# Kernel tuning notes

Measured on AMD Instinct MI355X. Metric: run time of the kernel, lower is better.

Reference implementation:

```python
import jax, jax.numpy as jnp
import numpy as np

N_NODES = 4096
N_EDGES = 16384
F_IN = 64
F_EDGE = 16
HID = 128
OUT = 64
N_GRAPHS = 32


def _encoder(x, edge_index, edge_attr, batch, p):
    N = x.shape[0]
    src, dst = edge_index[0], edge_index[1]
    # EdgeMLP: [E, F_edge] -> [E, F_in * HID] per-edge weight matrices
    h = jax.nn.relu(edge_attr @ p['e_w1'] + p['e_b1'])
    h = jax.nn.relu(h @ p['e_w2'] + p['e_b2'])
    Wmat = (h @ p['e_w3'] + p['e_b3']).reshape(-1, x.shape[1], p['root_w'].shape[1])  # [E, F_in, HID]
    # NNConv: message = x_src @ W_edge, scatter-add to dst, plus root transform + bias
    msg = jnp.einsum('ei,eio->eo', x[src], Wmat)  # [E, HID]
    agg = jax.ops.segment_sum(msg, dst, num_segments=N)
    h1 = jax.nn.relu(agg + x @ p['root_w'] + p['conv1_b'])  # [N, HID]
    # GATConv (1 head, concat=False) with self-loops (PyG default)
    loop = jnp.arange(N, dtype=src.dtype)
    si = jnp.concatenate([src, loop])
    di = jnp.concatenate([dst, loop])
    hp = h1 @ p['gat_w']  # [N, HID]
    a_s = hp @ p['att_src']  # [N]
    a_d = hp @ p['att_dst']  # [N]
    e = jax.nn.leaky_relu(a_s[si] + a_d[di], negative_slope=0.2)
    m = jax.ops.segment_max(e, di, num_segments=N)
    ex = jnp.exp(e - m[di])
    denom = jax.ops.segment_sum(ex, di, num_segments=N)
    alpha = ex / (denom[di] + 1e-16)
    h2 = jax.ops.segment_sum(alpha[:, None] * hp[si], di, num_segments=N) + p['gat_b']
    h2 = jax.nn.relu(h2)
    # global mean pool over graphs
    s = jax.ops.segment_sum(h2, batch, num_segments=N_GRAPHS)
    cnt = jax.ops.segment_sum(jnp.ones((N,), h2.dtype), batch, num_segments=N_GRAPHS)
    pooled = s / jnp.maximum(cnt, 1.0)[:, None]
    return jax.nn.relu(pooled @ p['fc1_w'] + p['fc1_b'])  # [B, OUT]


def setup_inputs() -> dict:
    key = jax.random.key(0)
    ks = jax.random.split(key, 24)
    d = {}
    d['x1'] = jax.random.normal(ks[0], (N_NODES, F_IN), jnp.float32)
    d['edge_index1'] = jax.random.randint(ks[1], (2, N_EDGES), 0, N_NODES)
    d['edge_attr1'] = jax.random.normal(ks[2], (N_EDGES, F_EDGE), jnp.float32)
    d['batch1'] = jnp.sort(jax.random.randint(ks[3], (N_NODES,), 0, N_GRAPHS))
    d['x2'] = jax.random.normal(ks[4], (N_NODES, F_IN), jnp.float32)
    d['edge_index2'] = jax.random.randint(ks[5], (2, N_EDGES), 0, N_NODES)
    d['edge_attr2'] = jax.random.normal(ks[6], (N_EDGES, F_EDGE), jnp.float32)
    d['batch2'] = jnp.sort(jax.random.randint(ks[7], (N_NODES,), 0, N_GRAPHS))

    def lin(k, fi, fo):
        return jax.random.normal(k, (fi, fo), jnp.float32) * (fi ** -0.5)

    d['e_w1'] = lin(ks[8], F_EDGE, 128); d['e_b1'] = jnp.zeros((128,), jnp.float32)
    d['e_w2'] = lin(ks[9], 128, 64); d['e_b2'] = jnp.zeros((64,), jnp.float32)
    d['e_w3'] = lin(ks[10], 64, F_IN * HID); d['e_b3'] = jnp.zeros((F_IN * HID,), jnp.float32)
    d['root_w'] = lin(ks[11], F_IN, HID); d['conv1_b'] = jnp.zeros((HID,), jnp.float32)
    d['gat_w'] = lin(ks[12], HID, HID)
    d['att_src'] = jax.random.normal(ks[13], (HID,), jnp.float32) * (HID ** -0.5)
    d['att_dst'] = jax.random.normal(ks[14], (HID,), jnp.float32) * (HID ** -0.5)
    d['gat_b'] = jnp.zeros((HID,), jnp.float32)
    d['fc1_w'] = lin(ks[15], HID, OUT); d['fc1_b'] = jnp.zeros((OUT,), jnp.float32)
    d['fc2_w'] = lin(ks[16], OUT, 1); d['fc2_b'] = jnp.zeros((1,), jnp.float32)
    return d


def reference(x1, edge_index1, edge_attr1, batch1, x2, edge_index2, edge_attr2, batch2,
              e_w1, e_b1, e_w2, e_b2, e_w3, e_b3, root_w, conv1_b,
              gat_w, att_src, att_dst, gat_b, fc1_w, fc1_b, fc2_w, fc2_b):
    p = dict(e_w1=e_w1, e_b1=e_b1, e_w2=e_w2, e_b2=e_b2, e_w3=e_w3, e_b3=e_b3,
             root_w=root_w, conv1_b=conv1_b, gat_w=gat_w, att_src=att_src,
             att_dst=att_dst, gat_b=gat_b, fc1_w=fc1_w, fc1_b=fc1_b,
             fc2_w=fc2_w, fc2_b=fc2_b)
    z1 = _encoder(x1, edge_index1, edge_attr1, batch1, p)
    z2 = _encoder(x2, edge_index2, edge_attr2, batch2, p)
    z = jnp.abs(z1 - z2) @ fc2_w + fc2_b  # [B, 1]
    return jax.nn.sigmoid(z).squeeze(1)  # [B]
```

## Files before the change

### kernel.cpp

```cpp
#include <hip/hip_runtime.h>
#include <hip/hip_bf16.h>
#include <math.h>

#define NN 4096
#define NE 16384
#define FIN 64
#define FE 16
#define HIDD 128
#define OUTD 64
#define NG 32
#define EP (NE + NN)
#define KSPLIT 2
#define NCH (64 / KSPLIT)

typedef __attribute__((ext_vector_type(4))) unsigned u4v;
typedef __attribute__((ext_vector_type(4))) float f4v;
typedef _Float16 f16x8 __attribute__((ext_vector_type(8)));

union FragH { u4v u; f16x8 h; };
union FH2 { _Float16 f[2]; unsigned u; };
union F16x8U { _Float16 f[8]; u4v u; };

__global__ void k_splitB(const float* __restrict__ w3, unsigned short* __restrict__ B1t) {
    __shared__ float lds[64 * 129];
    int c = blockIdx.x, t = threadIdx.x;
#pragma unroll
    for (int r = 0; r < 32; ++r) {
        int idx = r * 256 + t;
        lds[(idx >> 7) * 129 + (idx & 127)] = w3[(size_t)c * 8192 + idx];
    }
    __syncthreads();
#pragma unroll
    for (int r = 0; r < 32; ++r) {
        int e = r * 256 + t;
        float v = lds[(e & 63) * 129 + (e >> 6)];
        union { _Float16 f; unsigned short u; } cv;
        cv.f = (_Float16)v;
        B1t[(size_t)c * 8192 + e] = cv.u;
    }
}

#define PB_EMLP  4096
#define PB_BIAS  (PB_EMLP + 4096)
#define PB_TOTAL (PB_BIAS + 32)

__global__ void k_prep(const float* __restrict__ ea0, const float* __restrict__ ea1,
                       const float* __restrict__ w1, const float* __restrict__ b1,
                       const float* __restrict__ w2, const float* __restrict__ b2,
                       const float* __restrict__ X0, const float* __restrict__ X1,
                       const float* __restrict__ b3,
                       const int* __restrict__ ei0, const int* __restrict__ ei1,
                       float* __restrict__ h0, float* __restrict__ h1g,
                       float* __restrict__ Bb0, float* __restrict__ Bb1,
                       int* __restrict__ rowcnt) {
    int b = blockIdx.x, t = threadIdx.x;
    if (b < PB_EMLP) {
        int gi = b >> 11;
        int e0 = (b & 2047) * 8;
        const float* ea = gi ? ea1 : ea0;
        float* hout = gi ? h1g : h0;
        __shared__ float h1s[8][HIDD];
#pragma unroll
        for (int r = 0; r < 4; ++r) {
            int idx = r * 256 + t;
            int e1 = idx >> 7, j = idx & 127;
            float acc = b1[j];
#pragma unroll
            for (int i = 0; i < FE; ++i) acc += ea[(e0 + e1) * FE + i] * w1[i * HIDD + j];
            h1s[e1][j] = fmaxf(acc, 0.f);
        }
        __syncthreads();
#pragma unroll
        for (int r = 0; r < 2; ++r) {
            int idx = r * 256 + t;
            int e1 = idx >> 6, j = idx & 63;
            float acc = b2[j];
#pragma unroll 16
            for (int k = 0; k < HIDD; ++k) acc += h1s[e1][k] * w2[k * 64 + j];
            hout[(size_t)(e0 + e1) * 64 + j] = fmaxf(acc, 0.f);
        }
    } else if (b < PB_BIAS) {
        int bb = b - PB_EMLP;
        int gi = bb >> 11;
        int n = (bb & 2047) * 2 + (t >> 7);
        int o = t & 127;
        const float* X = gi ? X1 : X0;
        float* Bb = gi ? Bb1 : Bb0;
        float acc = 0.f;
#pragma unroll 16
        for (int i = 0; i < FIN; ++i) acc += X[n * FIN + i] * b3[i * HIDD + o];
        Bb[(size_t)n * HIDD + o] = acc;
    } else {
        int tid = (b - PB_BIAS) * 256 + t;
        for (int idx = tid; idx < 2 * EP; idx += 32 * 256) {
            int gi = idx / EP, e = idx % EP;
            const int* dst = (gi ? ei1 : ei0) + NE;
            int d = (e < NE) ? dst[e] : e - NE;
            atomicAdd(&rowcnt[gi * NN + d], 1);
        }
    }
}

__global__ void k_scan(const int* __restrict__ rowcnt, int* __restrict__ rowptr,
                       const int* __restrict__ batch0, const int* __restrict__ batch1,
                       int* __restrict__ br) {
    int b = blockIdx.x;
    if (b < 2) {
        int gi = b;
        const int* cnt = rowcnt + gi * NN;
        int* rp = rowptr + gi * (NN + 1);
        int t = threadIdx.x;
        int base = t * 4;
        int v0 = cnt[base], v1 = cnt[base + 1], v2 = cnt[base + 2], v3 = cnt[base + 3];
        int s = v0 + v1 + v2 + v3;
        __shared__ int sc[1024];
        sc[t] = s;
        __syncthreads();
        for (int off = 1; off < 1024; off <<= 1) {
            int a = (t >= off) ? sc[t - off] : 0;
            __syncthreads();
            sc[t] += a;
            __syncthreads();
        }
        int run = sc[t] - s;
        rp[base] = run; run += v0;
        rp[base + 1] = run; run += v1;
        rp[base + 2] = run; run += v2;
        rp[base + 3] = run; run += v3;
        if (t == 1023) rp[NN] = run;
    } else {
        int t = threadIdx.x;
        if (t < 66) {
            int gi = t / 33, g = t % 33;
            const int* batch = gi ? batch1 : batch0;
            int lo = 0, hi = NN;
            while (lo < hi) {
                int mid = (lo + hi) >> 1;
                if (batch[mid] < g) lo = mid + 1; else hi = mid;
            }
            br[gi * 33 + g] = lo;
        }
    }
}

__global__ void k_fill(const int* __restrict__ ei0, const int* __restrict__ ei1,
                       const int* __restrict__ rowptr, int* __restrict__ cnt2,
                       int* __restrict__ adj) {
    int idx = blockIdx.x * 256 + threadIdx.x;
    if (idx >= 2 * EP) return;
    int gi = idx / EP, e = idx % EP;
    const int* dst = (gi ? ei1 : ei0) + NE;
    int d = (e < NE) ? dst[e] : e - NE;
    int pos = rowptr[gi * (NN + 1) + d] + atomicAdd(&cnt2[gi * NN + d], 1);
    adj[gi * EP + pos] = e;
}

__global__ void __launch_bounds__(128, 2)
k_nnconv(const float* __restrict__ x0, const float* __restrict__ x1,
         const float* __restrict__ h_0, const float* __restrict__ h_1,
         const unsigned short* __restrict__ B1t,
         const float* __restrict__ Bb0, const float* __restrict__ Bb1,
         const int* __restrict__ ei0, const int* __restrict__ ei1,
         _Float16* __restrict__ msgh) {
    __shared__ __align__(16) float sm[32 * 128];
    int gi = blockIdx.z;
    const float* x = gi ? x1 : x0;
    const float* hh = gi ? h_1 : h_0;
    const float* Bb = gi ? Bb1 : Bb0;
    const int* src = gi ? ei1 : ei0;

    int t = threadIdx.x;
    int e0 = blockIdx.x * 64;
    int z = blockIdx.y;
    int ch = t >> 6;
    int l = t & 63, q4 = l >> 4, c16 = l & 15;

    FragH xf[4][2];
#pragma unroll
    for (int mf = 0; mf < 4; ++mf) {
        int s_ = src[e0 + mf * 16 + c16];
        const float* xr = &x[(size_t)s_ * FIN];
#pragma unroll
        for (int kf = 0; kf < 2; ++kf) {
            float xv[8];
            *(float4*)&xv[0] = *(const float4*)&xr[kf * 32 + q4 * 8];
            *(float4*)&xv[4] = *(const float4*)&xr[kf * 32 + q4 * 8 + 4];
            u4v w;
#pragma unroll
            for (int p = 0; p < 4; ++p) {
                FH2 c2;
                c2.f[0] = (_Float16)xv[2 * p];
                c2.f[1] = (_Float16)xv[2 * p + 1];
                w[p] = c2.u;
            }
            xf[mf][kf].u = w;
        }
    }

    f4v acc[4][4];
#pragma unroll
    for (int a = 0; a < 4; ++a)
#pragma unroll
        for (int b = 0; b < 4; ++b) acc[a][b] = (f4v){0.f, 0.f, 0.f, 0.f};

    const u4v* bp = (const u4v*)B1t;

#define LOADF(buf, cg)                                                          \
    {                                                                           \
        const u4v* cp = bp + (size_t)(cg) * 1024;                               \
        _Pragma("unroll") for (int kf = 0; kf < 2; ++kf)                        \
        _Pragma("unroll") for (int nf = 0; nf < 4; ++nf)                        \
            buf[kf * 4 + nf].u = cp[(ch * 64 + nf * 16 + c16) * 8 + kf * 4 + q4]; \
    }

#define DOMFMA(buf, COMP)                                                       \
    {                                                                           \
        _Pragma("unroll") for (int mf = 0; mf < 4; ++mf) {                      \
            FH2 hp2;                                                            \
            hp2.f[0] = (_Float16)hv4[mf].COMP;                                  \
            hp2.f[1] = hp2.f[0];                                                \
            unsigned hw = hp2.u;                                                \
            FragH hb; hb.u = (u4v){hw, hw, hw, hw};                             \
            _Pragma("unroll") for (int kf = 0; kf < 2; ++kf) {                  \
                FragH a1;                                                       \
                a1.h = hb.h * xf[mf][kf].h;                                     \
                _Pragma("unroll") for (int nf = 0; nf < 4; ++nf) {              \
                    acc[mf][nf] = __builtin_amdgcn_mfma_f32_16x16x32_f16(       \
                        a1.h, buf[kf * 4 + nf].h, acc[mf][nf], 0, 0, 0);        \
                }                                                               \
            }                                                                   \
        }                                                                       \
    }

    FragH bA[8], bB[8];
    float4 hv4[4];
    LOADF(bA, z * NCH);
#pragma unroll 1
    for (int cl = 0; cl < NCH; cl += 4) {
#pragma unroll
        for (int mf = 0; mf < 4; ++mf)
            hv4[mf] = *(const float4*)&hh[(size_t)(e0 + mf * 16 + c16) * 64 + z * NCH + cl];
        LOADF(bB, z * NCH + cl + 1);
        DOMFMA(bA, x);
        LOADF(bA, z * NCH + cl + 2);
        DOMFMA(bB, y);
        LOADF(bB, z * NCH + cl + 3);
        DOMFMA(bA, z);
        if (cl + 4 < NCH) LOADF(bA, z * NCH + cl + 4);
        DOMFMA(bB, w);
    }
#undef LOADF
#undef DOMFMA

    _Float16* mb = msgh + (size_t)(gi * KSPLIT + z) * NE * HIDD;
    int z0 = (z == 0);
#pragma unroll
    for (int half = 0; half < 2; ++half) {
        if (half) __syncthreads();
#pragma unroll
        for (int mf2 = 0; mf2 < 2; ++mf2) {
            int mf = half * 2 + mf2;
#pragma unroll
            for (int j = 0; j < 4; ++j) {
                int rr = mf2 * 16 + q4 * 4 + j;
#pragma unroll
                for (int nf = 0; nf < 4; ++nf)
                    sm[rr * 128 + ch * 64 + nf * 16 + c16] = acc[mf][nf][j];
            }
        }
        __syncthreads();
#pragma unroll
        for (int it = 0; it < 4; ++it) {
            int u = it * 128 + t;
            int row = u >> 4, c8 = u & 15;
            int eg = e0 + half * 32 + row;
            float v[8];
            *(float4*)&v[0] = *(float4*)&sm[row * 128 + c8 * 8];
            *(float4*)&v[4] = *(float4*)&sm[row * 128 + c8 * 8 + 4];
            if (z0) {
                int s_ = src[eg];
                const float* bbr = &Bb[(size_t)s_ * HIDD + c8 * 8];
#pragma unroll
                for (int j = 0; j < 8; ++j) v[j] += bbr[j];
            }
            F16x8U cv;
#pragma unroll
            for (int j = 0; j < 8; ++j) cv.f[j] = (_Float16)v[j];
            *(u4v*)&mb[(size_t)eg * HIDD + c8 * 8] = cv.u;
        }
    }
}

__global__ void k_h1hp(const _Float16* __restrict__ msgh,
                       const int* __restrict__ rowptr, const int* __restrict__ adj,
                       const float* __restrict__ X0, const float* __restrict__ X1,
                       const float* __restrict__ rw, const float* __restrict__ cb,
                       const float* __restrict__ gw,
                       const float* __restrict__ asw, const float* __restrict__ adw,
                       float* __restrict__ hp0, float* __restrict__ hp1,
                       float* __restrict__ a_s0, float* __restrict__ a_s1,
                       float* __restrict__ a_d0, float* __restrict__ a_d1) {
    int gi = blockIdx.y;
    const float* X = gi ? X1 : X0;
    float* hp = gi ? hp1 : hp0;
    float* a_s = gi ? a_s1 : a_s0;
    float* a_d = gi ? a_d1 : a_d0;
    const int* rp = rowptr + gi * (NN + 1);
    const int* aj = adj + gi * EP;
    const _Float16* m0 = msgh + (size_t)(gi * KSPLIT + 0) * NE * HIDD;
    const _Float16* m1 = msgh + (size_t)(gi * KSPLIT + 1) * NE * HIDD;
    int n0 = blockIdx.x * 16;
    int t = threadIdx.x;
    int o = t & 127, q = t >> 7;
    __shared__ float xsh[16][FIN];
    __shared__ float h1s[16][HIDD];
    __shared__ float s1[16][2], s2[16][2];
#pragma unroll
    for (int r = 0; r < 2; ++r) {
        int idx = r * 512 + t;
        xsh[idx >> 6][idx & 63] = X[(n0 + (idx >> 6)) * FIN + (idx & 63)];
    }
    __syncthreads();
    float accs[4];
#pragma unroll
    for (int nn = 0; nn < 4; ++nn) {
        int n = n0 + q * 4 + nn;
        float acc = cb[o];
        int lo = rp[n], hi = rp[n + 1];
        for (int p = lo; p < hi; ++p) {
            int e = aj[p];
            if (e < NE) {
                size_t eo = (size_t)e * HIDD + o;
                acc += (float)m0[eo] + (float)m1[eo];
            }
        }
        accs[nn] = acc;
    }
#pragma unroll 8
    for (int i = 0; i < FIN; ++i) {
        float w = rw[i * HIDD + o];
#pragma unroll
        for (int nn = 0; nn < 4; ++nn) accs[nn] += xsh[q * 4 + nn][i] * w;
    }
#pragma unroll
    for (int nn = 0; nn < 4; ++nn) h1s[q * 4 + nn][o] = fmaxf(accs[nn], 0.f);
    __syncthreads();
#pragma unroll
    for (int nn = 0; nn < 4; ++nn) accs[nn] = 0.f;
#pragma unroll 8
    for (int k = 0; k < HIDD; ++k) {
        float w = gw[k * HIDD + o];
#pragma unroll
        for (int nn = 0; nn < 4; ++nn) accs[nn] += h1s[q * 4 + nn][k] * w;
    }
#pragma unroll
    for (int nn = 0; nn < 4; ++nn) {
        int n = n0 + q * 4 + nn;
        hp[(size_t)n * HIDD + o] = accs[nn];
        float p1 = accs[nn] * asw[o], p2 = accs[nn] * adw[o];
#pragma unroll
        for (int off = 32; off; off >>= 1) {
            p1 += __shfl_down(p1, off);
            p2 += __shfl_down(p2, off);
        }
        if ((o & 63) == 0) { s1[q * 4 + nn][o >> 6] = p1; s2[q * 4 + nn][o >> 6] = p2; }
    }
    __syncthreads();
    if (t < 16) {
        a_s[n0 + t] = s1[t][0] + s1[t][1];
        a_d[n0 + t] = s2[t][0] + s2[t][1];
    }
}

__global__ void k_gat(const int* __restrict__ rowptr, const int* __restrict__ adj,
                      const int* __restrict__ ei0, const int* __restrict__ ei1,
                      const float* __restrict__ hp0, const float* __restrict__ hp1,
                      const float* __restrict__ as0, const float* __restrict__ as1,
                      const float* __restrict__ ad0, const float* __restrict__ ad1,
                      const float* __restrict__ gb,
                      float* __restrict__ h2_0, float* __restrict__ h2_1) {
    int gi = blockIdx.y;
    const int* src = gi ? ei1 : ei0;
    const float* hp = gi ? hp1 : hp0;
    const float* a_s = gi ? as1 : as0;
    const float* a_d = gi ? ad1 : ad0;
    float* h2 = gi ? h2_1 : h2_0;
    const int* rp = rowptr + gi * (NN + 1);
    const int* aj = adj + gi * EP;
    int w = threadIdx.x >> 6, l = threadIdx.x & 63;
    int n = blockIdx.x * 4 + w;
    int lo = rp[n], deg = rp[n + 1] - lo;
    float adn = a_d[n];
    float m = -1e30f;
    for (int base = 0; base < deg; base += 64) {
        float sc = -1e30f;
        int j = base + l;
        if (j < deg) {
            int e = aj[lo + j];
            int si = (e < NE) ? src[e] : n;
            float xsc = a_s[si] + adn;
            sc = xsc > 0.f ? xsc : 0.2f * xsc;
        }
#pragma unroll
        for (int off = 32; off; off >>= 1) sc = fmaxf(sc, __shfl_xor(sc, off));
        m = fmaxf(m, sc);
    }
    float den = 0.f;
    for (int base = 0; base < deg; base += 64) {
        float ev = 0.f;
        int j = base + l;
        if (j < deg) {
            int e = aj[lo + j];
            int si = (e < NE) ? src[e] : n;
            float xsc = a_s[si] + adn;
            float sc = xsc > 0.f ? xsc : 0.2f * xsc;
            ev = expf(sc - m);
        }
#pragma unroll
        for (int off = 32; off; off >>= 1) ev += __shfl_xor(ev, off);
        den += ev;
    }
    float inv = 1.f / (den + 1e-16f);
    float acc0 = 0.f, acc1 = 0.f;
    for (int j = 0; j < deg; ++j) {
        int e = aj[lo + j];
        int si = (e < NE) ? src[e] : n;
        float xsc = a_s[si] + adn;
        float sc = xsc > 0.f ? xsc : 0.2f * xsc;
        float al = expf(sc - m) * inv;
        acc0 += al * hp[(size_t)si * HIDD + l];
        acc1 += al * hp[(size_t)si * HIDD + 64 + l];
    }
    h2[(size_t)n * HIDD + l] = fmaxf(acc0 + gb[l], 0.f);
    h2[(size_t)n * HIDD + 64 + l] = fmaxf(acc1 + gb[64 + l], 0.f);
}

__global__ void k_poolfc1(const float* __restrict__ h2_0, const float* __restrict__ h2_1,
                          const int* __restrict__ br,
                          const float* __restrict__ w, const float* __restrict__ bias,
                          float* __restrict__ z) {
    int gi = blockIdx.x >> 5, g = blockIdx.x & 31;
    const float* h2 = gi ? h2_1 : h2_0;
    int lo = br[gi * 33 + g], hi = br[gi * 33 + g + 1];
    int t = threadIdx.x;
    __shared__ float pool[HIDD];
    float acc = 0.f;
    for (int n = lo; n < hi; ++n) acc += h2[(size_t)n * HIDD + t];
    pool[t] = acc;
    __syncthreads();
    if (t < 64) {
        float c = fmaxf((float)(hi - lo), 1.f);
        float a = bias[t];
#pragma unroll 16
        for (int o = 0; o < HIDD; ++o) a += (pool[o] / c) * w[o * OUTD + t];
        z[gi * NG * OUTD + g * OUTD + t] = fmaxf(a, 0.f);
    }
}

__global__ void k_final(const float* __restrict__ zz,
                        const float* __restrict__ w, const float* __restrict__ b,
                        float* __restrict__ out) {
    int g = threadIdx.x;
    const float* z1 = zz;
    const float* z2 = zz + NG * OUTD;
    float acc = b[0];
#pragma unroll
    for (int j = 0; j < OUTD; ++j) acc += fabsf(z1[g * OUTD + j] - z2[g * OUTD + j]) * w[j];
    out[g] = 1.f / (1.f + expf(-acc));
}

extern "C" void kernel_launch(void* const* d_in, const int* in_sizes, int n_in,
                              void* d_out, int out_size, void* d_ws, size_t ws_size,
                              hipStream_t stream) {
    const float* x0     = (const float*)d_in[0];
    const int*   ei0    = (const int*)d_in[1];
    const float* ea0    = (const float*)d_in[2];
    const int*   b0     = (const int*)d_in[3];
    const float* x1     = (const float*)d_in[4];
    const int*   ei1    = (const int*)d_in[5];
    const float* ea1    = (const float*)d_in[6];
    const int*   b1     = (const int*)d_in[7];
    const float* e_w1 = (const float*)d_in[8];
    const float* e_b1 = (const float*)d_in[9];
    const float* e_w2 = (const float*)d_in[10];
    const float* e_b2 = (const float*)d_in[11];
    const float* e_w3 = (const float*)d_in[12];
    const float* e_b3 = (const float*)d_in[13];
    const float* root_w = (const float*)d_in[14];
    const float* conv1_b = (const float*)d_in[15];
    const float* gat_w = (const float*)d_in[16];
    const float* att_src = (const float*)d_in[17];
    const float* att_dst = (const float*)d_in[18];
    const float* gat_b = (const float*)d_in[19];
    const float* fc1_w = (const float*)d_in[20];
    const float* fc1_b = (const float*)d_in[21];
    const float* fc2_w = (const float*)d_in[22];
    const float* fc2_b = (const float*)d_in[23];

    float* ws = (float*)d_ws;
    size_t off = 0;
    auto alloc = [&](size_t n) { float* p = ws + off; off += n; return p; };
    int* rowcnt = (int*)alloc(2 * NN);
    int* cnt2   = (int*)alloc(2 * NN);
    size_t zero_elems = off;
    int* rowptr = (int*)alloc(2 * (NN + 1));
    int* br     = (int*)alloc(66);
    int* adj    = (int*)alloc(2 * EP);
    float* h[2]   = {alloc((size_t)NE * 64), alloc((size_t)NE * 64)};
    unsigned short* B1t = (unsigned short*)alloc((size_t)4096 * 128 / 2);
    float* Bb[2]  = {alloc((size_t)NN * HIDD), alloc((size_t)NN * HIDD)};
    _Float16* msgh = (_Float16*)alloc((size_t)2 * KSPLIT * NE * HIDD / 2);
    float* hp[2]  = {alloc((size_t)NN * HIDD), alloc((size_t)NN * HIDD)};
    float* a_s[2] = {alloc(NN), alloc(NN)};
    float* a_d[2] = {alloc(NN), alloc(NN)};
    float* h2[2]  = {alloc((size_t)NN * HIDD), alloc((size_t)NN * HIDD)};
    float* zz     = alloc((size_t)2 * NG * OUTD);

    (void)hipMemsetAsync(ws, 0, zero_elems * 4, stream);
    k_splitB<<<64, 256, 0, stream>>>(e_w3, B1t);
    k_prep<<<PB_TOTAL, 256, 0, stream>>>(ea0, ea1, e_w1, e_b1, e_w2, e_b2,
                                         x0, x1, e_b3, ei0, ei1,
                                         h[0], h[1], Bb[0], Bb[1],
                                         rowcnt);
    k_scan<<<3, 1024, 0, stream>>>(rowcnt, rowptr, b0, b1, br);
    k_fill<<<(2 * EP + 255) / 256, 256, 0, stream>>>(ei0, ei1, rowptr, cnt2, adj);
    k_nnconv<<<dim3(NE / 64, KSPLIT, 2), 128, 0, stream>>>(
        x0, x1, h[0], h[1], B1t, Bb[0], Bb[1], ei0, ei1, msgh);
    k_h1hp<<<dim3(NN / 16, 2), 512, 0, stream>>>(
        msgh, rowptr, adj, x0, x1, root_w, conv1_b, gat_w, att_src, att_dst,
        hp[0], hp[1], a_s[0], a_s[1], a_d[0], a_d[1]);
    k_gat<<<dim3(NN / 4, 2), 256, 0, stream>>>(
        rowptr, adj, ei0, ei1, hp[0], hp[1], a_s[0], a_s[1], a_d[0], a_d[1],
        gat_b, h2[0], h2[1]);
    k_poolfc1<<<64, HIDD, 0, stream>>>(h2[0], h2[1], br, fc1_w, fc1_b, zz);
    k_final<<<1, NG, 0, stream>>>(zz, fc2_w, fc2_b, (float*)d_out);
}
```

Baseline: 243.0 us.

## Fold weight split into prep kernel, warp-shuffle scan, triple-buffer NNConv loads

Moves the e_w3 transpose/fp16 conversion into extra blocks of the prep kernel, which removes one kernel launch. Replaces the LDS Hillis-Steele scan that synchronises on every step with a wave-shuffle scan plus a 16-entry cross-wave pass. In the NNConv kernel, the weight fragments are now triple-buffered with a prefetch distance of 3, and the per-edge h values are loaded as scalars one chunk ahead instead of as float4 per four chunks. The third buffer raises register pressure, and the large static LDS array in the prep kernel may lower occupancy for the other prep blocks.

```diff
diff --git a/kernel.cpp b/kernel.cpp
--- a/kernel.cpp
+++ b/kernel.cpp
@@ -21,35 +21,19 @@
 union FH2 { _Float16 f[2]; unsigned u; };
 union F16x8U { _Float16 f[8]; u4v u; };
 
-__global__ void k_splitB(const float* __restrict__ w3, unsigned short* __restrict__ B1t) {
-    __shared__ float lds[64 * 129];
-    int c = blockIdx.x, t = threadIdx.x;
-#pragma unroll
-    for (int r = 0; r < 32; ++r) {
-        int idx = r * 256 + t;
-        lds[(idx >> 7) * 129 + (idx & 127)] = w3[(size_t)c * 8192 + idx];
-    }
-    __syncthreads();
-#pragma unroll
-    for (int r = 0; r < 32; ++r) {
-        int e = r * 256 + t;
-        float v = lds[(e & 63) * 129 + (e >> 6)];
-        union { _Float16 f; unsigned short u; } cv;
-        cv.f = (_Float16)v;
-        B1t[(size_t)c * 8192 + e] = cv.u;
-    }
-}
-
 #define PB_EMLP  4096
 #define PB_BIAS  (PB_EMLP + 4096)
-#define PB_TOTAL (PB_BIAS + 32)
+#define PB_HIST  (PB_BIAS + 32)
+#define PB_TOTAL (PB_HIST + 64)
 
 __global__ void k_prep(const float* __restrict__ ea0, const float* __restrict__ ea1,
                        const float* __restrict__ w1, const float* __restrict__ b1,
                        const float* __restrict__ w2, const float* __restrict__ b2,
+                       const float* __restrict__ w3,
                        const float* __restrict__ X0, const float* __restrict__ X1,
                        const float* __restrict__ b3,
                        const int* __restrict__ ei0, const int* __restrict__ ei1,
+                       unsigned short* __restrict__ B1t,
                        float* __restrict__ h0, float* __restrict__ h1g,
                        float* __restrict__ Bb0, float* __restrict__ Bb1,
                        int* __restrict__ rowcnt) {
@@ -90,13 +74,30 @@
 #pragma unroll 16
         for (int i = 0; i < FIN; ++i) acc += X[n * FIN + i] * b3[i * HIDD + o];
         Bb[(size_t)n * HIDD + o] = acc;
-    } else {
+    } else if (b < PB_HIST) {
         int tid = (b - PB_BIAS) * 256 + t;
         for (int idx = tid; idx < 2 * EP; idx += 32 * 256) {
             int gi = idx / EP, e = idx % EP;
             const int* dst = (gi ? ei1 : ei0) + NE;
             int d = (e < NE) ? dst[e] : e - NE;
             atomicAdd(&rowcnt[gi * NN + d], 1);
+        }
+    } else {
+        __shared__ float lds[64 * 129];
+        int c = b - PB_HIST;
+#pragma unroll
+        for (int r = 0; r < 32; ++r) {
+            int idx = r * 256 + t;
+            lds[(idx >> 7) * 129 + (idx & 127)] = w3[(size_t)c * 8192 + idx];
+        }
+        __syncthreads();
+#pragma unroll
+        for (int r = 0; r < 32; ++r) {
+            int e = r * 256 + t;
+            float v = lds[(e & 63) * 129 + (e >> 6)];
+            union { _Float16 f; unsigned short u; } cv;
+            cv.f = (_Float16)v;
+            B1t[(size_t)c * 8192 + e] = cv.u;
         }
     }
 }
@@ -110,19 +111,31 @@
         const int* cnt = rowcnt + gi * NN;
         int* rp = rowptr + gi * (NN + 1);
         int t = threadIdx.x;
+        int lane = t & 63, w = t >> 6;
         int base = t * 4;
         int v0 = cnt[base], v1 = cnt[base + 1], v2 = cnt[base + 2], v3 = cnt[base + 3];
         int s = v0 + v1 + v2 + v3;
-        __shared__ int sc[1024];
-        sc[t] = s;
+        int inc = s;
+#pragma unroll
+        for (int off = 1; off < 64; off <<= 1) {
+            int u = __shfl_up(inc, off);
+            if (lane >= off) inc += u;
+        }
+        __shared__ int wsum[16];
+        if (lane == 63) wsum[w] = inc;
         __syncthreads();
-        for (int off = 1; off < 1024; off <<= 1) {
-            int a = (t >= off) ? sc[t - off] : 0;
-            __syncthreads();
-            sc[t] += a;
-            __syncthreads();
-        }
-        int run = sc[t] - s;
+        if (t < 16) {
+            int ws = wsum[t];
+            int wi = ws;
+#pragma unroll
+            for (int off = 1; off < 16; off <<= 1) {
+                int u = __shfl_up(wi, off);
+                if (t >= off) wi += u;
+            }
+            wsum[t] = wi - ws;
+        }
+        __syncthreads();
+        int run = wsum[w] + inc - s;
         rp[base] = run; run += v0;
         rp[base + 1] = run; run += v1;
         rp[base + 2] = run; run += v2;
@@ -176,9 +189,11 @@
     int l = t & 63, q4 = l >> 4, c16 = l & 15;
 
     FragH xf[4][2];
+    int hb_[4];
 #pragma unroll
     for (int mf = 0; mf < 4; ++mf) {
         int s_ = src[e0 + mf * 16 + c16];
+        hb_[mf] = (e0 + mf * 16 + c16) * 64 + z * NCH;
         const float* xr = &x[(size_t)s_ * FIN];
 #pragma unroll
         for (int kf = 0; kf < 2; ++kf) {
@@ -213,42 +228,55 @@
             buf[kf * 4 + nf].u = cp[(ch * 64 + nf * 16 + c16) * 8 + kf * 4 + q4]; \
     }
 
-#define DOMFMA(buf, COMP)                                                       \
+#define DOMFMA(buf)                                                             \
     {                                                                           \
         _Pragma("unroll") for (int mf = 0; mf < 4; ++mf) {                      \
             FH2 hp2;                                                            \
-            hp2.f[0] = (_Float16)hv4[mf].COMP;                                  \
+            hp2.f[0] = (_Float16)hvC[mf];                                       \
             hp2.f[1] = hp2.f[0];                                                \
             unsigned hw = hp2.u;                                                \
             FragH hb; hb.u = (u4v){hw, hw, hw, hw};                             \
             _Pragma("unroll") for (int kf = 0; kf < 2; ++kf) {                  \
                 FragH a1;                                                       \
                 a1.h = hb.h * xf[mf][kf].h;                                     \
-                _Pragma("unroll") for (int nf = 0; nf < 4; ++nf) {              \
+                _Pragma("unroll") for (int nf = 0; nf < 4; ++nf)                \
                     acc[mf][nf] = __builtin_amdgcn_mfma_f32_16x16x32_f16(       \
                         a1.h, buf[kf * 4 + nf].h, acc[mf][nf], 0, 0, 0);        \
-                }                                                               \
             }                                                                   \
         }                                                                       \
     }
 
-    FragH bA[8], bB[8];
-    float4 hv4[4];
-    LOADF(bA, z * NCH);
+#define STAGE(buf, cl, DO_H, DO_L)                                              \
+    {                                                                           \
+        if (DO_H) {                                                             \
+            _Pragma("unroll") for (int mf = 0; mf < 4; ++mf)                    \
+                hvN[mf] = hh[hb_[mf] + (cl) + 1];                               \
+        }                                                                       \
+        DOMFMA(buf);                                                            \
+        if (DO_L) LOADF(buf, z * NCH + (cl) + 3);                               \
+        _Pragma("unroll") for (int mf = 0; mf < 4; ++mf) hvC[mf] = hvN[mf];     \
+    }
+
+    FragH bA[8], bB[8], bC[8];
+    float hvC[4], hvN[4];
+    LOADF(bA, z * NCH + 0);
+    LOADF(bB, z * NCH + 1);
+    LOADF(bC, z * NCH + 2);
+#pragma unroll
+    for (int mf = 0; mf < 4; ++mf) hvC[mf] = hh[hb_[mf]];
+
 #pragma unroll 1
-    for (int cl = 0; cl < NCH; cl += 4) {
-#pragma unroll
-        for (int mf = 0; mf < 4; ++mf)
-            hv4[mf] = *(const float4*)&hh[(size_t)(e0 + mf * 16 + c16) * 64 + z * NCH + cl];
-        LOADF(bB, z * NCH + cl + 1);
-        DOMFMA(bA, x);
-        LOADF(bA, z * NCH + cl + 2);
-        DOMFMA(bB, y);
-        LOADF(bB, z * NCH + cl + 3);
-        DOMFMA(bA, z);
-        if (cl + 4 < NCH) LOADF(bA, z * NCH + cl + 4);
-        DOMFMA(bB, w);
-    }
+    for (int cl = 0; cl < NCH - 5; cl += 3) {
+        STAGE(bA, cl, 1, 1);
+        STAGE(bB, cl + 1, 1, 1);
+        STAGE(bC, cl + 2, 1, 1);
+    }
+    STAGE(bA, NCH - 5, 1, 1);
+    STAGE(bB, NCH - 4, 1, 1);
+    STAGE(bC, NCH - 3, 1, 0);
+    STAGE(bA, NCH - 2, 1, 0);
+    STAGE(bB, NCH - 1, 0, 0);
+#undef STAGE
 #undef LOADF
 #undef DOMFMA
 
@@ -517,10 +545,9 @@
     float* zz     = alloc((size_t)2 * NG * OUTD);
 
     (void)hipMemsetAsync(ws, 0, zero_elems * 4, stream);
-    k_splitB<<<64, 256, 0, stream>>>(e_w3, B1t);
-    k_prep<<<PB_TOTAL, 256, 0, stream>>>(ea0, ea1, e_w1, e_b1, e_w2, e_b2,
+    k_prep<<<PB_TOTAL, 256, 0, stream>>>(ea0, ea1, e_w1, e_b1, e_w2, e_b2, e_w3,
                                          x0, x1, e_b3, ei0, ei1,
-                                         h[0], h[1], Bb[0], Bb[1],
+                                         B1t, h[0], h[1], Bb[0], Bb[1],
                                          rowcnt);
     k_scan<<<3, 1024, 0, stream>>>(rowcnt, rowptr, b0, b1, br);
     k_fill<<<(2 * EP + 255) / 256, 256, 0, stream>>>(ei0, ei1, rowptr, cnt2, adj);
```

After: 245.9 us. No clear change (+1.2%).

## Fold weight transpose into prep kernel, use wave-shuffle scan, raise MFMA priority

Applied to the files above, without the earlier changes.

The standalone k_splitB launch is merged into k_prep as 64 extra blocks, removing one kernel launch and letting the transpose overlap with the other prep work. The row-pointer scan replaces a 10-step LDS Hillis-Steele loop, which has two barriers per step, with a wave shuffle scan followed by a small cross-wave scan. The MFMA section of the NNConv kernel is wrapped in s_setprio so waves issuing matrix ops get scheduling priority over waves doing loads. Merging the kernels adds a 33KB shared array to every k_prep block, which may reduce occupancy for the EMLP and bias branches.

```diff
diff --git a/kernel.cpp b/kernel.cpp
--- a/kernel.cpp
+++ b/kernel.cpp
@@ -21,35 +21,19 @@
 union FH2 { _Float16 f[2]; unsigned u; };
 union F16x8U { _Float16 f[8]; u4v u; };
 
-__global__ void k_splitB(const float* __restrict__ w3, unsigned short* __restrict__ B1t) {
-    __shared__ float lds[64 * 129];
-    int c = blockIdx.x, t = threadIdx.x;
-#pragma unroll
-    for (int r = 0; r < 32; ++r) {
-        int idx = r * 256 + t;
-        lds[(idx >> 7) * 129 + (idx & 127)] = w3[(size_t)c * 8192 + idx];
-    }
-    __syncthreads();
-#pragma unroll
-    for (int r = 0; r < 32; ++r) {
-        int e = r * 256 + t;
-        float v = lds[(e & 63) * 129 + (e >> 6)];
-        union { _Float16 f; unsigned short u; } cv;
-        cv.f = (_Float16)v;
-        B1t[(size_t)c * 8192 + e] = cv.u;
-    }
-}
-
 #define PB_EMLP  4096
 #define PB_BIAS  (PB_EMLP + 4096)
-#define PB_TOTAL (PB_BIAS + 32)
+#define PB_HIST  (PB_BIAS + 32)
+#define PB_TOTAL (PB_HIST + 64)
 
 __global__ void k_prep(const float* __restrict__ ea0, const float* __restrict__ ea1,
                        const float* __restrict__ w1, const float* __restrict__ b1,
                        const float* __restrict__ w2, const float* __restrict__ b2,
+                       const float* __restrict__ w3,
                        const float* __restrict__ X0, const float* __restrict__ X1,
                        const float* __restrict__ b3,
                        const int* __restrict__ ei0, const int* __restrict__ ei1,
+                       unsigned short* __restrict__ B1t,
                        float* __restrict__ h0, float* __restrict__ h1g,
                        float* __restrict__ Bb0, float* __restrict__ Bb1,
                        int* __restrict__ rowcnt) {
@@ -90,13 +74,30 @@
 #pragma unroll 16
         for (int i = 0; i < FIN; ++i) acc += X[n * FIN + i] * b3[i * HIDD + o];
         Bb[(size_t)n * HIDD + o] = acc;
-    } else {
+    } else if (b < PB_HIST) {
         int tid = (b - PB_BIAS) * 256 + t;
         for (int idx = tid; idx < 2 * EP; idx += 32 * 256) {
             int gi = idx / EP, e = idx % EP;
             const int* dst = (gi ? ei1 : ei0) + NE;
             int d = (e < NE) ? dst[e] : e - NE;
             atomicAdd(&rowcnt[gi * NN + d], 1);
+        }
+    } else {
+        __shared__ float lds[64 * 129];
+        int c = b - PB_HIST;
+#pragma unroll
+        for (int r = 0; r < 32; ++r) {
+            int idx = r * 256 + t;
+            lds[(idx >> 7) * 129 + (idx & 127)] = w3[(size_t)c * 8192 + idx];
+        }
+        __syncthreads();
+#pragma unroll
+        for (int r = 0; r < 32; ++r) {
+            int e = r * 256 + t;
+            float v = lds[(e & 63) * 129 + (e >> 6)];
+            union { _Float16 f; unsigned short u; } cv;
+            cv.f = (_Float16)v;
+            B1t[(size_t)c * 8192 + e] = cv.u;
         }
     }
 }
@@ -110,19 +111,31 @@
         const int* cnt = rowcnt + gi * NN;
         int* rp = rowptr + gi * (NN + 1);
         int t = threadIdx.x;
+        int lane = t & 63, w = t >> 6;
         int base = t * 4;
         int v0 = cnt[base], v1 = cnt[base + 1], v2 = cnt[base + 2], v3 = cnt[base + 3];
         int s = v0 + v1 + v2 + v3;
-        __shared__ int sc[1024];
-        sc[t] = s;
+        int inc = s;
+#pragma unroll
+        for (int off = 1; off < 64; off <<= 1) {
+            int u = __shfl_up(inc, off);
+            if (lane >= off) inc += u;
+        }
+        __shared__ int wsum[16];
+        if (lane == 63) wsum[w] = inc;
         __syncthreads();
-        for (int off = 1; off < 1024; off <<= 1) {
-            int a = (t >= off) ? sc[t - off] : 0;
-            __syncthreads();
-            sc[t] += a;
-            __syncthreads();
-        }
-        int run = sc[t] - s;
+        if (t < 16) {
+            int ws = wsum[t];
+            int wi = ws;
+#pragma unroll
+            for (int off = 1; off < 16; off <<= 1) {
+                int u = __shfl_up(wi, off);
+                if (t >= off) wi += u;
+            }
+            wsum[t] = wi - ws;
+        }
+        __syncthreads();
+        int run = wsum[w] + inc - s;
         rp[base] = run; run += v0;
         rp[base + 1] = run; run += v1;
         rp[base + 2] = run; run += v2;
@@ -215,6 +228,7 @@
 
 #define DOMFMA(buf, COMP)                                                       \
     {                                                                           \
+        __builtin_amdgcn_s_setprio(1);                                          \
         _Pragma("unroll") for (int mf = 0; mf < 4; ++mf) {                      \
             FH2 hp2;                                                            \
             hp2.f[0] = (_Float16)hv4[mf].COMP;                                  \
@@ -230,6 +244,7 @@
                 }                                                               \
             }                                                                   \
         }                                                                       \
+        __builtin_amdgcn_s_setprio(0);                                          \
     }
 
     FragH bA[8], bB[8];
@@ -517,10 +532,9 @@
     float* zz     = alloc((size_t)2 * NG * OUTD);
 
     (void)hipMemsetAsync(ws, 0, zero_elems * 4, stream);
-    k_splitB<<<64, 256, 0, stream>>>(e_w3, B1t);
-    k_prep<<<PB_TOTAL, 256, 0, stream>>>(ea0, ea1, e_w1, e_b1, e_w2, e_b2,
+    k_prep<<<PB_TOTAL, 256, 0, stream>>>(ea0, ea1, e_w1, e_b1, e_w2, e_b2, e_w3,
                                          x0, x1, e_b3, ei0, ei1,
-                                         h[0], h[1], Bb[0], Bb[1],
+                                         B1t, h[0], h[1], Bb[0], Bb[1],
                                          rowcnt);
     k_scan<<<3, 1024, 0, stream>>>(rowcnt, rowptr, b0, b1, br);
     k_fill<<<(2 * EP + 255) / 256, 256, 0, stream>>>(ei0, ei1, rowptr, cnt2, adj);
```

Result: no change. 239.9 us, median of 3 (-1.3%).
